# Performance work log

Hardware: AMD Instinct MI355X
Metric: run time of the kernel (lower is better)

Reference implementation:

```python
import jax, jax.numpy as jnp
import numpy as np

# Static config (matches init_kwargs)
B, H, W, C = 16, 64, 64, 512
HEADS, WS, SHIFT = 16, 8, 4
N = WS * WS                      # tokens per window = 64
NW = (H // WS) * (W // WS)       # windows per image = 64
HID = 4 * C                      # MLP hidden = 2048
HEAD_DIM = C // HEADS
SCALE = HEAD_DIM ** -0.5
EPS = 1e-5


def _layer_norm(x, w, b):
    m = jnp.mean(x, axis=-1, keepdims=True)
    v = jnp.mean((x - m) ** 2, axis=-1, keepdims=True)
    return (x - m) / jnp.sqrt(v + EPS) * w + b


def _rel_pos_idx():
    coords = np.stack(np.meshgrid(np.arange(WS), np.arange(WS), indexing='ij')).reshape(2, -1)
    rel = coords[:, :, None] - coords[:, None, :]          # (2, N, N)
    rel = rel.transpose(1, 2, 0)                           # (N, N, 2)
    rel[:, :, 0] += WS - 1
    rel[:, :, 1] += WS - 1
    rel[:, :, 0] *= 2 * WS - 1
    return rel.sum(-1)                                     # (N, N) int


def _attn_mask():
    img = np.zeros((H, W), dtype=np.float32)
    sls = (slice(0, -WS), slice(-WS, -SHIFT), slice(-SHIFT, None))
    cnt = 0
    for hs in sls:
        for ws_ in sls:
            img[hs, ws_] = cnt
            cnt += 1
    # window partition (H,W) -> (NW, N)
    mw = img.reshape(H // WS, WS, W // WS, WS).transpose(0, 2, 1, 3).reshape(-1, N)
    diff = mw[:, None, :] - mw[:, :, None]                 # (NW, N, N)
    return np.where(diff != 0, -100.0, 0.0).astype(np.float32)


def setup_inputs() -> dict:
    key = jax.random.key(0)
    ks = jax.random.split(key, 8)
    s = 0.02
    return {
        'x': jax.random.normal(ks[0], (B, H * W, C), jnp.float32),
        'qkv_w': jax.random.normal(ks[1], (3 * C, C), jnp.float32) * s,
        'qkv_b': jnp.zeros((3 * C,), jnp.float32),
        'proj_w': jax.random.normal(ks[2], (C, C), jnp.float32) * s,
        'proj_b': jnp.zeros((C,), jnp.float32),
        'norm1_w': jnp.ones((C,), jnp.float32),
        'norm1_b': jnp.zeros((C,), jnp.float32),
        'norm2_w': jnp.ones((C,), jnp.float32),
        'norm2_b': jnp.zeros((C,), jnp.float32),
        'fc1_w': jax.random.normal(ks[3], (HID, C), jnp.float32) * s,
        'fc1_b': jnp.zeros((HID,), jnp.float32),
        'fc2_w': jax.random.normal(ks[4], (C, HID), jnp.float32) * s,
        'fc2_b': jnp.zeros((C,), jnp.float32),
        'rel_bias_table': jax.random.normal(ks[5], ((2 * WS - 1) ** 2, HEADS), jnp.float32) * s,
        'rel_pos_idx': jnp.asarray(_rel_pos_idx(), jnp.int32),
        'attn_mask': jnp.asarray(_attn_mask(), jnp.float32),
    }


def _swin_block(x, qkv_w, qkv_b, proj_w, proj_b, norm1_w, norm1_b,
                norm2_w, norm2_b, fc1_w, fc1_b, fc2_w, fc2_b,
                rel_bias_table, rel_pos_idx, attn_mask):
    Bx = x.shape[0]
    shortcut = x
    h = _layer_norm(x, norm1_w, norm1_b).reshape(Bx, H, W, C)
    h = jnp.roll(h, (-SHIFT, -SHIFT), axis=(1, 2))
    # window partition -> (B*NW, N, C)
    h = h.reshape(Bx, H // WS, WS, W // WS, WS, C).transpose(0, 1, 3, 2, 4, 5)
    h = h.reshape(Bx * NW, N, C)
    # qkv projection
    qkv = h @ qkv_w.T + qkv_b                               # (B_, N, 3C)
    qkv = qkv.reshape(Bx * NW, N, 3, HEADS, HEAD_DIM).transpose(2, 0, 3, 1, 4)
    q, k, v = qkv[0], qkv[1], qkv[2]                        # (B_, heads, N, hd)
    attn = jnp.einsum('bhnd,bhmd->bhnm', q, k) * SCALE      # (B_, heads, N, N)
    rp_bias = rel_bias_table[rel_pos_idx]                   # (N, N, heads)
    attn = attn + rp_bias.transpose(2, 0, 1)[None]
    # shift mask (per window)
    attn = attn.reshape(Bx, NW, HEADS, N, N) + attn_mask[None, :, None]
    attn = jax.nn.softmax(attn.reshape(Bx * NW, HEADS, N, N), axis=-1)
    o = jnp.einsum('bhnm,bhmd->bhnd', attn, v)              # (B_, heads, N, hd)
    o = o.transpose(0, 2, 1, 3).reshape(Bx * NW, N, C)
    o = o @ proj_w.T + proj_b
    # window reverse -> (B, H, W, C)
    o = o.reshape(Bx, H // WS, W // WS, WS, WS, C).transpose(0, 1, 3, 2, 4, 5)
    o = o.reshape(Bx, H, W, C)
    o = jnp.roll(o, (SHIFT, SHIFT), axis=(1, 2))
    x = shortcut + o.reshape(Bx, H * W, C)
    # MLP
    h2 = _layer_norm(x, norm2_w, norm2_b)
    h2 = jax.nn.gelu(h2 @ fc1_w.T + fc1_b, approximate=False)
    return x + (h2 @ fc2_w.T + fc2_b)


def reference(x, qkv_w, qkv_b, proj_w, proj_b, norm1_w, norm1_b,
              norm2_w, norm2_b, fc1_w, fc1_b, fc2_w, fc2_b,
              rel_bias_table, rel_pos_idx, attn_mask):
    return _swin_block(x, qkv_w, qkv_b, proj_w, proj_b, norm1_w, norm1_b,
                       norm2_w, norm2_b, fc1_w, fc1_b, fc2_w, fc2_b,
                       rel_bias_table, rel_pos_idx, attn_mask)
```

## Files before the change

kernel.cpp:

```cpp
#include <hip/hip_runtime.h>
#include <hip/hip_bf16.h>

typedef __attribute__((ext_vector_type(8))) short short8;
typedef __attribute__((ext_vector_type(4))) float f32x4;

__device__ __forceinline__ short f2bfbits(float f) {
  union { __hip_bfloat16 h; short s; } cvt;
  cvt.h = __float2bfloat16(f);
  return cvt.s;
}
__device__ __forceinline__ float bfbits2f(short bits) {
  union { unsigned int u; float f; } cvt;
  cvt.u = ((unsigned int)(unsigned short)bits) << 16;
  return cvt.f;
}

__device__ __forceinline__ void gl_lds16(const short* g, short* l) {
  __builtin_amdgcn_global_load_lds(
      (__attribute__((address_space(1))) void*)(g),
      (__attribute__((address_space(3))) void*)(l), 16, 0, 0);
}

__global__ __launch_bounds__(256)
void f2bf4(const float* __restrict__ s0, short* __restrict__ d0,
           const float* __restrict__ s1, short* __restrict__ d1,
           const float* __restrict__ s2, short* __restrict__ d2,
           const float* __restrict__ s3, short* __restrict__ d3) {
  const int bi = blockIdx.x;
  const float* s; short* d; int b;
  if (bi < 768)       { s = s0; d = d0; b = bi; }
  else if (bi < 1024) { s = s1; d = d1; b = bi - 768; }
  else if (bi < 2048) { s = s2; d = d2; b = bi - 1024; }
  else                { s = s3; d = d3; b = bi - 2048; }
  const int i = (b * 256 + threadIdx.x) * 4;
  float4 v = *(const float4*)(s + i);
  short o[4] = {f2bfbits(v.x), f2bfbits(v.y), f2bfbits(v.z), f2bfbits(v.w)};
  *(uint2*)(d + i) = *(const uint2*)o;
}

__global__ __launch_bounds__(256)
void bm_build(const float* __restrict__ table, const int* __restrict__ idx,
              const float* __restrict__ mask, short* __restrict__ bm) {
  const int wi = blockIdx.x, hh = blockIdx.y;
  const int n = threadIdx.x & 63;
  const int m0 = (threadIdx.x >> 6) * 16;
#pragma unroll
  for (int mm = 0; mm < 16; mm++) {
    const int m = m0 + mm;
    const float t = table[idx[m * 64 + n] * 16 + hh];
    const float mk = mask[wi * 4096 + m * 64 + n];
    bm[((long)(wi * 16 + hh) * 64 + m) * 64 + n] = f2bfbits(t + mk);
  }
}

__global__ __launch_bounds__(256)
void ln1_win(const float* __restrict__ x, const float* __restrict__ w,
             const float* __restrict__ b, short* __restrict__ h) {
  const int lane = threadIdx.x & 63;
  const int wv = threadIdx.x >> 6;
  const int t = blockIdx.x * 4 + wv;
  const int n = t & 63, wiB = t >> 6;
  const int wi = wiB & 63, bb = wiB >> 6;
  const int sr = (((wi >> 3) << 3) + (n >> 3) + 4) & 63;
  const int sc = (((wi & 7) << 3) + (n & 7) + 4) & 63;
  const float* xp = x + ((long)bb * 4096 + sr * 64 + sc) * 512 + lane * 8;
  float4 u0 = *(const float4*)(xp);
  float4 u1 = *(const float4*)(xp + 4);
  float v[8] = {u0.x, u0.y, u0.z, u0.w, u1.x, u1.y, u1.z, u1.w};
  float s = 0.f;
#pragma unroll
  for (int j = 0; j < 8; j++) s += v[j];
#pragma unroll
  for (int o = 1; o < 64; o <<= 1) s += __shfl_xor(s, o, 64);
  const float mean = s * (1.0f / 512.0f);
  float q = 0.f;
#pragma unroll
  for (int j = 0; j < 8; j++) { float d = v[j] - mean; q += d * d; }
#pragma unroll
  for (int o = 1; o < 64; o <<= 1) q += __shfl_xor(q, o, 64);
  const float rstd = rsqrtf(q * (1.0f / 512.0f) + 1e-5f);
  float4 w0 = *(const float4*)(w + lane * 8);
  float4 w1 = *(const float4*)(w + lane * 8 + 4);
  float4 b0 = *(const float4*)(b + lane * 8);
  float4 b1 = *(const float4*)(b + lane * 8 + 4);
  const float wv8[8] = {w0.x, w0.y, w0.z, w0.w, w1.x, w1.y, w1.z, w1.w};
  const float bv8[8] = {b0.x, b0.y, b0.z, b0.w, b1.x, b1.y, b1.z, b1.w};
  short outs[8];
#pragma unroll
  for (int j = 0; j < 8; j++)
    outs[j] = f2bfbits((v[j] - mean) * rstd * wv8[j] + bv8[j]);
  *(uint4*)(h + (long)t * 512 + lane * 8) = *(const uint4*)outs;
}

__global__ __launch_bounds__(256)
void ln2_id(const float* __restrict__ x2, const float* __restrict__ w,
            const float* __restrict__ b, short* __restrict__ out) {
  const int lane = threadIdx.x & 63;
  const int wv = threadIdx.x >> 6;
  const long t = blockIdx.x * 4 + wv;
  const float* xp = x2 + t * 512 + lane * 8;
  float4 u0 = *(const float4*)(xp);
  float4 u1 = *(const float4*)(xp + 4);
  float v[8] = {u0.x, u0.y, u0.z, u0.w, u1.x, u1.y, u1.z, u1.w};
  float s = 0.f;
#pragma unroll
  for (int j = 0; j < 8; j++) s += v[j];
#pragma unroll
  for (int o = 1; o < 64; o <<= 1) s += __shfl_xor(s, o, 64);
  const float mean = s * (1.0f / 512.0f);
  float q = 0.f;
#pragma unroll
  for (int j = 0; j < 8; j++) { float d = v[j] - mean; q += d * d; }
#pragma unroll
  for (int o = 1; o < 64; o <<= 1) q += __shfl_xor(q, o, 64);
  const float rstd = rsqrtf(q * (1.0f / 512.0f) + 1e-5f);
  float4 w0 = *(const float4*)(w + lane * 8);
  float4 w1 = *(const float4*)(w + lane * 8 + 4);
  float4 b0 = *(const float4*)(b + lane * 8);
  float4 b1 = *(const float4*)(b + lane * 8 + 4);
  const float wv8[8] = {w0.x, w0.y, w0.z, w0.w, w1.x, w1.y, w1.z, w1.w};
  const float bv8[8] = {b0.x, b0.y, b0.z, b0.w, b1.x, b1.y, b1.z, b1.w};
  short outs[8];
#pragma unroll
  for (int j = 0; j < 8; j++)
    outs[j] = f2bfbits((v[j] - mean) * rstd * wv8[j] + bv8[j]);
  *(uint4*)(out + t * 512 + lane * 8) = *(const uint4*)outs;
}

template <int MODE, int K, int GN>
__global__ __launch_bounds__(256, 2)
void gemm128(const short* __restrict__ A, const short* __restrict__ Bw,
             const float* __restrict__ bias, const float* __restrict__ aux,
             void* __restrict__ outv, short* __restrict__ out2) {
  __shared__ short lds[32768];
  constexpr int NT = K / 64;
  const int tid = threadIdx.x;
  const int lane = tid & 63, wave = tid >> 6;
  const int l15 = lane & 15, quad = lane >> 4;
  const int wr = wave >> 1, wc = wave & 1;

  const int nwg = gridDim.x;
  const int chunk = nwg >> 3;
  const int wg = (blockIdx.x & 7) * chunk + (blockIdx.x >> 3);
  const int row0 = (wg / GN) * 128;
  const int col0 = (wg % GN) * 128;

  const int srow = lane >> 3;
  const int scol = ((lane & 7) ^ srow) * 8;
  const short* Ag = A + (long)(row0 + wave * 32 + srow) * K + scol;
  const short* Bg = Bw + (long)(col0 + wave * 32 + srow) * K + scol;
  short* ldsAw = lds + wave * 2048;
  short* ldsBw = lds + 16384 + wave * 2048;

  const int g0 = (quad ^ (l15 & 7)) * 8;
  const int g1 = ((quad ^ 4) ^ (l15 & 7)) * 8;
  const int aB0 = (wr * 64 + l15) * 64 + g0;
  const int aB1 = (wr * 64 + l15) * 64 + g1;
  const int bB0 = 16384 + (wc * 64 + l15) * 64 + g0;
  const int bB1 = 16384 + (wc * 64 + l15) * 64 + g1;
  const int aBF = wr ? aB1 : aB0, aBS = wr ? aB0 : aB1;
  const int bBF = wr ? bB1 : bB0, bBS = wr ? bB0 : bB1;

  f32x4 acc[4][4];
#pragma unroll
  for (int m = 0; m < 4; m++)
#pragma unroll
    for (int n = 0; n < 4; n++) acc[m][n] = (f32x4){0.f, 0.f, 0.f, 0.f};

#define STAGE(cOff, kt)                                               \
  {                                                                   \
    const short* a_ = Ag + (kt) * 64;                                 \
    const short* b_ = Bg + (kt) * 64;                                 \
    _Pragma("unroll") for (int i_ = 0; i_ < 4; i_++) {                \
      gl_lds16(a_ + (long)i_ * 8 * K, ldsAw + (cOff) + i_ * 512);     \
      gl_lds16(b_ + (long)i_ * 8 * K, ldsBw + (cOff) + i_ * 512);     \
    }                                                                 \
  }

  STAGE(0, 0);
  STAGE(8192, 1);
  asm volatile("s_waitcnt vmcnt(8)" ::: "memory");
  __builtin_amdgcn_s_barrier();

  for (int t = 0; t < NT; ++t) {
    const int c = (t & 1) << 13;
    short8 AF[4], BF[4], AS[4], BS[4];

#pragma unroll
    for (int n = 0; n < 4; n++) BF[n] = *(const short8*)(lds + c + bBF + n * 1024);
#pragma unroll
    for (int m = 0; m < 4; m++) AF[m] = *(const short8*)(lds + c + aBF + m * 1024);
    __builtin_amdgcn_s_setprio(1);
#pragma unroll
    for (int m = 0; m < 4; m++)
#pragma unroll
      for (int n = 0; n < 4; n++)
        acc[m][n] = __builtin_amdgcn_mfma_f32_16x16x32_bf16(AF[m], BF[n], acc[m][n], 0, 0, 0);
    __builtin_amdgcn_s_setprio(0);

#pragma unroll
    for (int m = 0; m < 4; m++) AS[m] = *(const short8*)(lds + c + aBS + m * 1024);
#pragma unroll
    for (int n = 0; n < 4; n++) BS[n] = *(const short8*)(lds + c + bBS + n * 1024);
    asm volatile("s_waitcnt lgkmcnt(0)" ::: "memory");
    asm volatile("s_waitcnt vmcnt(0)" ::: "memory");
    __builtin_amdgcn_s_barrier();
    if (t + 2 < NT) STAGE(c, t + 2);

    __builtin_amdgcn_s_setprio(1);
#pragma unroll
    for (int m = 0; m < 4; m++)
#pragma unroll
      for (int n = 0; n < 4; n++)
        acc[m][n] = __builtin_amdgcn_mfma_f32_16x16x32_bf16(AS[m], BS[n], acc[m][n], 0, 0, 0);
    __builtin_amdgcn_s_setprio(0);
  }
#undef STAGE

  const int rW = row0 + wr * 64;
  const int cW = col0 + wc * 64;
  if constexpr (MODE == 0) {
    if (col0 >= 1024) {
#pragma unroll
      for (int m = 0; m < 4; m++) {
        const int rbase = rW + m * 16 + quad * 4;
        const int w_ = rbase >> 6, tokb = rbase & 63;
#pragma unroll
        for (int n = 0; n < 4; n++) {
          const int col = cW + n * 16 + l15;
          const float bv = bias[col];
          const int cg = col - 1024;
          const int head = cg >> 5, d = cg & 31;
          short pk[4];
#pragma unroll
          for (int r = 0; r < 4; r++) pk[r] = f2bfbits(acc[m][n][r] + bv);
          *(uint2*)(out2 + ((long)(w_ * 16 + head) * 32 + d) * 64 + tokb) =
              *(const uint2*)pk;
        }
      }
    } else {
#pragma unroll
      for (int m = 0; m < 4; m++)
#pragma unroll
        for (int n = 0; n < 4; n++) {
          const int col = cW + n * 16 + l15;
          const float bv = bias[col];
#pragma unroll
          for (int r = 0; r < 4; r++) {
            const int row = rW + m * 16 + quad * 4 + r;
            ((short*)outv)[(long)row * 1024 + col] = f2bfbits(acc[m][n][r] + bv);
          }
        }
    }
  } else {
#pragma unroll
    for (int m = 0; m < 4; m++)
#pragma unroll
      for (int n = 0; n < 4; n++) {
        const int col = cW + n * 16 + l15;
        const float bv = bias[col];
#pragma unroll
        for (int r = 0; r < 4; r++) {
          const int row = rW + m * 16 + quad * 4 + r;
          float v = acc[m][n][r] + bv;
          if constexpr (MODE == 1) {
            const int n_ = row & 63, wiB = row >> 6;
            const int wi = wiB & 63, bb = wiB >> 6;
            const int p = (((wi >> 3) << 3) + (n_ >> 3) + 4) & 63;
            const int qq = (((wi & 7) << 3) + (n_ & 7) + 4) & 63;
            const long dst = ((long)bb * 4096 + p * 64 + qq) * 512 + col;
            ((float*)outv)[dst] = v + aux[dst];
          } else if constexpr (MODE == 2) {
            const float g = 0.5f * v * (1.0f + erff(v * 0.70710678118654752f));
            ((short*)outv)[(long)row * (GN * 128) + col] = f2bfbits(g);
          } else {
            const long ix = (long)row * (GN * 128) + col;
            ((float*)outv)[ix] = v + aux[ix];
          }
        }
      }
  }
}

__global__ __launch_bounds__(256)
void attn(const short* __restrict__ qk, const short* __restrict__ vT,
          const short* __restrict__ bm, short* __restrict__ o) {
  __shared__ short P[4][64 * 72];
  const int lane = threadIdx.x & 63, wave = threadIdx.x >> 6;
  const int l15 = lane & 15, quad = lane >> 4;
  const int w = blockIdx.x;
  const int hh = blockIdx.y * 4 + wave;
  const int wi = w & 63;
  const short* base = qk + (long)w * 64 * 1024;

  short8 qf[4], kf[4];
#pragma unroll
  for (int mt = 0; mt < 4; mt++) {
    const int tq = mt * 16 + l15;
    qf[mt] = *(const short8*)(base + tq * 1024 + hh * 32 + quad * 8);
    kf[mt] = *(const short8*)(base + tq * 1024 + 512 + hh * 32 + quad * 8);
  }
  f32x4 S[4][4];
#pragma unroll
  for (int i = 0; i < 4; i++)
#pragma unroll
    for (int j = 0; j < 4; j++) S[i][j] = (f32x4){0.f, 0.f, 0.f, 0.f};
#pragma unroll
  for (int mt = 0; mt < 4; mt++)
#pragma unroll
    for (int nt = 0; nt < 4; nt++)
      S[mt][nt] = __builtin_amdgcn_mfma_f32_16x16x32_bf16(qf[mt], kf[nt], S[mt][nt], 0, 0, 0);

  short* pw = P[wave];
  const short* bmp = bm + (long)(wi * 16 + hh) * 4096;
  const float scale = 0.17677669529663687f;
#pragma unroll
  for (int mt = 0; mt < 4; mt++) {
#pragma unroll
    for (int reg = 0; reg < 4; reg++) {
      const int m = mt * 16 + quad * 4 + reg;
      float vals[4];
#pragma unroll
      for (int nt = 0; nt < 4; nt++)
        vals[nt] = S[mt][nt][reg] * scale + bfbits2f(bmp[m * 64 + nt * 16 + l15]);
      float mx = fmaxf(fmaxf(vals[0], vals[1]), fmaxf(vals[2], vals[3]));
#pragma unroll
      for (int o_ = 1; o_ < 16; o_ <<= 1) mx = fmaxf(mx, __shfl_xor(mx, o_, 64));
      float e[4], sum = 0.f;
#pragma unroll
      for (int nt = 0; nt < 4; nt++) { e[nt] = __expf(vals[nt] - mx); sum += e[nt]; }
#pragma unroll
      for (int o_ = 1; o_ < 16; o_ <<= 1) sum += __shfl_xor(sum, o_, 64);
      const float inv = 1.0f / sum;
#pragma unroll
      for (int nt = 0; nt < 4; nt++)
        pw[m * 72 + nt * 16 + l15] = f2bfbits(e[nt] * inv);
    }
  }

  const short* vbase = vT + (long)(w * 16 + hh) * 2048;
  f32x4 O[4][2];
#pragma unroll
  for (int i = 0; i < 4; i++)
#pragma unroll
    for (int j = 0; j < 2; j++) O[i][j] = (f32x4){0.f, 0.f, 0.f, 0.f};
#pragma unroll
  for (int ks = 0; ks < 2; ks++) {
    short8 vf[2];
#pragma unroll
    for (int nt = 0; nt < 2; nt++)
      vf[nt] = *(const short8*)(vbase + (nt * 16 + l15) * 64 + ks * 32 + quad * 8);
#pragma unroll
    for (int mt = 0; mt < 4; mt++) {
      short8 pf = *(const short8*)(pw + (mt * 16 + l15) * 72 + ks * 32 + quad * 8);
#pragma unroll
      for (int nt = 0; nt < 2; nt++)
        O[mt][nt] = __builtin_amdgcn_mfma_f32_16x16x32_bf16(pf, vf[nt], O[mt][nt], 0, 0, 0);
    }
  }
#pragma unroll
  for (int mt = 0; mt < 4; mt++)
#pragma unroll
    for (int nt = 0; nt < 2; nt++)
#pragma unroll
      for (int reg = 0; reg < 4; reg++) {
        const int t = mt * 16 + quad * 4 + reg;
        const int d = nt * 16 + l15;
        o[((long)w * 64 + t) * 512 + hh * 32 + d] = f2bfbits(O[mt][nt][reg]);
      }
}

extern "C" void kernel_launch(void* const* d_in, const int* in_sizes, int n_in,
                              void* d_out, int out_size, void* d_ws, size_t ws_size,
                              hipStream_t stream) {
  const float* x      = (const float*)d_in[0];
  const float* qkv_w  = (const float*)d_in[1];
  const float* qkv_b  = (const float*)d_in[2];
  const float* proj_w = (const float*)d_in[3];
  const float* proj_b = (const float*)d_in[4];
  const float* n1w    = (const float*)d_in[5];
  const float* n1b    = (const float*)d_in[6];
  const float* n2w    = (const float*)d_in[7];
  const float* n2b    = (const float*)d_in[8];
  const float* fc1_w  = (const float*)d_in[9];
  const float* fc1_b  = (const float*)d_in[10];
  const float* fc2_w  = (const float*)d_in[11];
  const float* fc2_b  = (const float*)d_in[12];
  const float* table  = (const float*)d_in[13];
  const int*   idx    = (const int*)d_in[14];
  const float* mask   = (const float*)d_in[15];

  char* ws = (char*)d_ws;
  const long MB = 1048576L;
  short* wq  = (short*)(ws);
  short* wp  = wq + 786432;
  short* w1  = wp + 262144;
  short* w2  = w1 + 1048576;
  short* bm  = (short*)(ws + 8 * MB);
  short* h   = (short*)(ws + 17 * MB);
  short* o   = h;
  short* xn2 = h;
  short* qk  = (short*)(ws + 81 * MB);
  short* h2c = qk;
  short* vT  = (short*)(ws + 209 * MB);
  float* out = (float*)d_out;

  f2bf4<<<3072, 256, 0, stream>>>(qkv_w, wq, proj_w, wp, fc1_w, w1, fc2_w, w2);
  bm_build<<<dim3(64, 16), 256, 0, stream>>>(table, idx, mask, bm);

  ln1_win<<<16384, 256, 0, stream>>>(x, n1w, n1b, h);
  gemm128<0, 512, 12><<<6144, 256, 0, stream>>>(h, wq, qkv_b, nullptr, qk, vT);
  attn<<<dim3(1024, 4), 256, 0, stream>>>(qk, vT, bm, o);
  gemm128<1, 512, 4><<<2048, 256, 0, stream>>>(o, wp, proj_b, x, out, nullptr);
  ln2_id<<<16384, 256, 0, stream>>>(out, n2w, n2b, xn2);
  for (int c = 0; c < 2; c++) {
    const long ro = (long)c * 32768;
    gemm128<2, 512, 16><<<4096, 256, 0, stream>>>(
        xn2 + ro * 512, w1, fc1_b, nullptr, h2c, nullptr);
    gemm128<3, 2048, 4><<<1024, 256, 0, stream>>>(
        h2c, w2, fc2_b, out + ro * 512, out + ro * 512, nullptr);
  }
}
```

Measured before the change: 1.012 ms.

## Load GEMM B operand directly into registers, stage only A through LDS

Result: slower. 1.365 ms (+34.9%).

```diff
diff --git a/kernel.cpp b/kernel.cpp
--- a/kernel.cpp
+++ b/kernel.cpp
@@ -132,7 +132,7 @@
 void gemm128(const short* __restrict__ A, const short* __restrict__ Bw,
              const float* __restrict__ bias, const float* __restrict__ aux,
              void* __restrict__ outv, short* __restrict__ out2) {
-  __shared__ short lds[32768];
+  __shared__ short lds[16384];
   constexpr int NT = K / 64;
   const int tid = threadIdx.x;
   const int lane = tid & 63, wave = tid >> 6;
@@ -148,18 +148,14 @@
   const int srow = lane >> 3;
   const int scol = ((lane & 7) ^ srow) * 8;
   const short* Ag = A + (long)(row0 + wave * 32 + srow) * K + scol;
-  const short* Bg = Bw + (long)(col0 + wave * 32 + srow) * K + scol;
   short* ldsAw = lds + wave * 2048;
-  short* ldsBw = lds + 16384 + wave * 2048;
 
   const int g0 = (quad ^ (l15 & 7)) * 8;
   const int g1 = ((quad ^ 4) ^ (l15 & 7)) * 8;
   const int aB0 = (wr * 64 + l15) * 64 + g0;
   const int aB1 = (wr * 64 + l15) * 64 + g1;
-  const int bB0 = 16384 + (wc * 64 + l15) * 64 + g0;
-  const int bB1 = 16384 + (wc * 64 + l15) * 64 + g1;
-  const int aBF = wr ? aB1 : aB0, aBS = wr ? aB0 : aB1;
-  const int bBF = wr ? bB1 : bB0, bBS = wr ? bB0 : bB1;
+
+  const short* Bgl = Bw + (long)(col0 + wc * 64 + l15) * K + quad * 8;
 
   f32x4 acc[4][4];
 #pragma unroll
@@ -167,55 +163,65 @@
 #pragma unroll
     for (int n = 0; n < 4; n++) acc[m][n] = (f32x4){0.f, 0.f, 0.f, 0.f};
 
-#define STAGE(cOff, kt)                                               \
+#define STAGEA(cOff, kt)                                              \
   {                                                                   \
     const short* a_ = Ag + (kt) * 64;                                 \
-    const short* b_ = Bg + (kt) * 64;                                 \
-    _Pragma("unroll") for (int i_ = 0; i_ < 4; i_++) {                \
+    _Pragma("unroll") for (int i_ = 0; i_ < 4; i_++)                  \
       gl_lds16(a_ + (long)i_ * 8 * K, ldsAw + (cOff) + i_ * 512);     \
-      gl_lds16(b_ + (long)i_ * 8 * K, ldsBw + (cOff) + i_ * 512);     \
-    }                                                                 \
-  }
-
-  STAGE(0, 0);
-  STAGE(8192, 1);
-  asm volatile("s_waitcnt vmcnt(8)" ::: "memory");
+  }
+#define LOADB(dst, kt)                                                     \
+  {                                                                        \
+    _Pragma("unroll") for (int nt_ = 0; nt_ < 4; nt_++)                    \
+      _Pragma("unroll") for (int ks_ = 0; ks_ < 2; ks_++)                  \
+        dst[nt_ * 2 + ks_] = *(const short8*)(Bgl + (long)nt_ * 16 * K +   \
+                                              (kt) * 64 + ks_ * 32);       \
+  }
+#define KSTEP(t, BC, BN)                                                     \
+  {                                                                          \
+    const int c = ((t) & 1) << 13;                                           \
+    if ((t) + 1 < NT) LOADB(BN, (t) + 1);                                    \
+    short8 A0[4], A1[4];                                                     \
+    _Pragma("unroll") for (int m = 0; m < 4; m++)                            \
+      A0[m] = *(const short8*)(lds + c + aB0 + m * 1024);                    \
+    _Pragma("unroll") for (int m = 0; m < 4; m++)                            \
+      A1[m] = *(const short8*)(lds + c + aB1 + m * 1024);                    \
+    __builtin_amdgcn_s_setprio(1);                                           \
+    _Pragma("unroll") for (int m = 0; m < 4; m++)                            \
+      _Pragma("unroll") for (int n = 0; n < 4; n++)                          \
+        acc[m][n] = __builtin_amdgcn_mfma_f32_16x16x32_bf16(                 \
+            A0[m], BC[n * 2], acc[m][n], 0, 0, 0);                           \
+    __builtin_amdgcn_s_setprio(0);                                           \
+    asm volatile("s_waitcnt lgkmcnt(0)" ::: "memory");                       \
+    __builtin_amdgcn_s_barrier();                                            \
+    if ((t) + 2 < NT) STAGEA(c, (t) + 2);                                    \
+    __builtin_amdgcn_s_setprio(1);                                           \
+    _Pragma("unroll") for (int m = 0; m < 4; m++)                            \
+      _Pragma("unroll") for (int n = 0; n < 4; n++)                          \
+        acc[m][n] = __builtin_amdgcn_mfma_f32_16x16x32_bf16(                 \
+            A1[m], BC[n * 2 + 1], acc[m][n], 0, 0, 0);                       \
+    __builtin_amdgcn_s_setprio(0);                                           \
+    if ((t) + 2 < NT) {                                                      \
+      asm volatile("s_waitcnt vmcnt(12)" ::: "memory");                      \
+    } else if ((t) + 1 < NT) {                                               \
+      asm volatile("s_waitcnt vmcnt(8)" ::: "memory");                       \
+    }                                                                        \
+    __builtin_amdgcn_s_barrier();                                            \
+  }
+
+  short8 Bs0[8], Bs1[8];
+  STAGEA(0, 0);
+  STAGEA(8192, 1);
+  LOADB(Bs0, 0);
+  asm volatile("s_waitcnt vmcnt(12)" ::: "memory");
   __builtin_amdgcn_s_barrier();
 
-  for (int t = 0; t < NT; ++t) {
-    const int c = (t & 1) << 13;
-    short8 AF[4], BF[4], AS[4], BS[4];
-
-#pragma unroll
-    for (int n = 0; n < 4; n++) BF[n] = *(const short8*)(lds + c + bBF + n * 1024);
-#pragma unroll
-    for (int m = 0; m < 4; m++) AF[m] = *(const short8*)(lds + c + aBF + m * 1024);
-    __builtin_amdgcn_s_setprio(1);
-#pragma unroll
-    for (int m = 0; m < 4; m++)
-#pragma unroll
-      for (int n = 0; n < 4; n++)
-        acc[m][n] = __builtin_amdgcn_mfma_f32_16x16x32_bf16(AF[m], BF[n], acc[m][n], 0, 0, 0);
-    __builtin_amdgcn_s_setprio(0);
-
-#pragma unroll
-    for (int m = 0; m < 4; m++) AS[m] = *(const short8*)(lds + c + aBS + m * 1024);
-#pragma unroll
-    for (int n = 0; n < 4; n++) BS[n] = *(const short8*)(lds + c + bBS + n * 1024);
-    asm volatile("s_waitcnt lgkmcnt(0)" ::: "memory");
-    asm volatile("s_waitcnt vmcnt(0)" ::: "memory");
-    __builtin_amdgcn_s_barrier();
-    if (t + 2 < NT) STAGE(c, t + 2);
-
-    __builtin_amdgcn_s_setprio(1);
-#pragma unroll
-    for (int m = 0; m < 4; m++)
-#pragma unroll
-      for (int n = 0; n < 4; n++)
-        acc[m][n] = __builtin_amdgcn_mfma_f32_16x16x32_bf16(AS[m], BS[n], acc[m][n], 0, 0, 0);
-    __builtin_amdgcn_s_setprio(0);
-  }
-#undef STAGE
+  for (int tt = 0; tt < NT; tt += 2) {
+    KSTEP(tt, Bs0, Bs1);
+    KSTEP(tt + 1, Bs1, Bs0);
+  }
+#undef KSTEP
+#undef LOADB
+#undef STAGEA
 
   const int rW = row0 + wr * 64;
   const int cW = col0 + wc * 64;
```
